# Optimization experiments

Hardware: AMD Instinct MI355X
Metric: run time of the kernel (lower is better)

## Reference

```python
import jax, jax.numpy as jnp
import numpy as np

DIM = 4096
BATCH = 2048
K = 40  # int(DIM * 0.01)


def fhh(x):
    """Fused fast Walsh-Hadamard / Hartley butterfly (recursion over static sizes)."""
    n = x.shape[-1]
    if n == 1:
        return x
    half = n // 2
    left, right = x[..., :half], x[..., half:]
    h_sum = left + right
    h_diff = left - right
    h_diff2 = h_diff + jnp.roll(h_diff, shift=1, axis=-1)
    return jnp.concatenate([fhh(h_sum), fhh(h_diff2)], axis=-1)


def setup_inputs() -> dict:
    key = jax.random.key(0)
    k1, k2, k3 = jax.random.split(key, 3)
    x = jax.random.normal(k1, (BATCH, DIM), dtype=jnp.float32)
    spectral_weights = jnp.ones((DIM,), dtype=jnp.float32)
    engram_values = jax.random.normal(k2, (DIM, K), dtype=jnp.float32) * 0.01
    engram_indices = jax.random.randint(k3, (DIM, K), 0, DIM)
    return {"x": x, "spectral_weights": spectral_weights,
            "engram_values": engram_values, "engram_indices": engram_indices}


def reference(x, spectral_weights, engram_values, engram_indices):
    wave = fhh(x)  # [B, DIM]
    # low-rank (diagonal) path
    low_rank_out = wave * spectral_weights  # [B, DIM]
    # sparse gather path: wave[:, engram_indices] -> [B, DIM, K]
    selected = wave[:, engram_indices]
    sparse_out = jnp.einsum('bdk,dk->bd', selected, engram_values)
    processed = low_rank_out + sparse_out
    return fhh(processed) / DIM
```

## Files before the change

### kernel.cpp

```cpp
#include <hip/hip_runtime.h>

#define DIM   4096
#define BATCH 2048
#define KNZ   40
#define ROWS  8
#define TPB   512
#define DPT   (DIM / TPB)

typedef int i32x2 __attribute__((ext_vector_type(2)));

__device__ __forceinline__ float shflx(float v, int m) { return __shfl_xor(v, m, 64); }
__device__ __forceinline__ float shfls(float v, int s) { return __shfl(v, s, 64); }

__device__ __forceinline__ int swz8(int d) { return (d << 4) ^ ((d >> 2) & 0x1f0); }

__device__ __forceinline__ unsigned short bfp(float f) {
  unsigned u = __float_as_uint(f);
  u += 0x7fffu + ((u >> 16) & 1u);
  return (unsigned short)(u >> 16);
}
__device__ __forceinline__ float bfu(unsigned short h) { return __uint_as_float(((unsigned)h) << 16); }
__device__ __forceinline__ float blo(unsigned u) { return __uint_as_float(u << 16); }
__device__ __forceinline__ float bhi(unsigned u) { return __uint_as_float(u & 0xffff0000u); }

template<int CTRL>
__device__ __forceinline__ float dppf(float x) {
  int i = __float_as_int(x);
  return __int_as_float(__builtin_amdgcn_update_dpp(i, i, CTRL, 0xF, 0xF, false));
}

template<int HL>
__device__ __forceinline__ float bfly1(float self, bool up) {
#if __has_builtin(__builtin_amdgcn_permlane32_swap)
  if constexpr (HL == 32) {
    i32x2 rr = __builtin_amdgcn_permlane32_swap(__float_as_int(self), __float_as_int(self), false, false);
    float s = __int_as_float(rr.x) + __int_as_float(rr.y);
    return up ? (s - 2.0f * self) : s;
  }
#endif
#if __has_builtin(__builtin_amdgcn_permlane16_swap)
  if constexpr (HL == 16) {
    i32x2 rr = __builtin_amdgcn_permlane16_swap(__float_as_int(self), __float_as_int(self), false, false);
    float s = __int_as_float(rr.x) + __int_as_float(rr.y);
    return up ? (s - 2.0f * self) : s;
  }
#endif
  float pv;
  if constexpr (HL == 8)      pv = dppf<0x128>(self);
  else if constexpr (HL == 2) pv = dppf<0x4E>(self);
  else if constexpr (HL == 1) pv = dppf<0xB1>(self);
  else                        pv = shflx(self, HL);
  float s = self + pv;
  float d = up ? (pv - self) : (self - pv);
  return up ? d : s;
}

template<int H>
__device__ __forceinline__ void stage_inlane(float v[64]) {
#pragma unroll
  for (int o = 0; o < 64; o += 2 * H) {
    float dt[H];
#pragma unroll
    for (int i = 0; i < H; ++i) {
      float a = v[o + i], b = v[o + H + i];
      dt[i] = a - b;
      v[o + i] = a + b;
    }
#pragma unroll
    for (int i = H - 1; i >= 1; --i) v[o + H + i] = dt[i] + dt[i - 1];
    v[o + H] = dt[0] + dt[H - 1];
  }
}

template<int HL>
__device__ __forceinline__ void stage_xlane(float v[64], int lane) {
  const bool up = (lane & HL) != 0;
  const int srcl = ((lane & (HL - 1)) == 0) ? (lane | (HL - 1)) : (lane - 1);
#pragma unroll
  for (int r = 0; r < 64; ++r) v[r] = bfly1<HL>(v[r], up);
  float dw = shfls(v[63], srcl);
#pragma unroll
  for (int r = 63; r >= 1; --r) {
    float d2 = v[r] + v[r - 1];
    v[r] = up ? d2 : v[r];
  }
  float d2 = v[0] + dw;
  v[0] = up ? d2 : v[0];
}

__device__ __forceinline__ void fhh_regs(float v[64], int lane) {
  stage_xlane<32>(v, lane);
  stage_xlane<16>(v, lane);
  stage_xlane<8>(v, lane);
  stage_xlane<4>(v, lane);
  stage_xlane<2>(v, lane);
  stage_xlane<1>(v, lane);
  stage_inlane<32>(v);
  stage_inlane<16>(v);
  stage_inlane<8>(v);
  stage_inlane<4>(v);
  stage_inlane<2>(v);
  stage_inlane<1>(v);
}

__global__ __launch_bounds__(TPB, 2) void aleph_fused(
    const float* __restrict__ x, const float* __restrict__ sw,
    const float* __restrict__ V, const int* __restrict__ I,
    float* __restrict__ out) {
  __shared__ unsigned short lds[DIM * ROWS];
  char* lb = (char*)lds;
  const int t = threadIdx.x;
  const int w = t >> 6;
  const int lane = t & 63;
  const size_t row = (size_t)blockIdx.x * ROWS + w;

  float v[64];
  {
    const float4* xp = (const float4*)(x + row * DIM + (size_t)lane * 64);
#pragma unroll
    for (int i = 0; i < 16; ++i) {
      float4 f = xp[i];
      v[4 * i] = f.x; v[4 * i + 1] = f.y; v[4 * i + 2] = f.z; v[4 * i + 3] = f.w;
    }
  }
  fhh_regs(v, lane);

#pragma unroll
  for (int r = 0; r < 64; ++r)
    *(unsigned short*)(lb + swz8(64 * lane + r) + 2 * w) = bfp(v[r]);
  __syncthreads();

  float preg[DPT][ROWS];
#pragma unroll
  for (int ii = 0; ii < DPT; ++ii) {
    const int d = ii * TPB + t;
    const float swd = sw[d];
    uint4 q = *(const uint4*)(lb + swz8(d));
    float a0 = blo(q.x) * swd, a1 = bhi(q.x) * swd;
    float a2 = blo(q.y) * swd, a3 = bhi(q.y) * swd;
    float a4 = blo(q.z) * swd, a5 = bhi(q.z) * swd;
    float a6 = blo(q.w) * swd, a7 = bhi(q.w) * swd;
    const int4*   ip = (const int4*)(I + d * KNZ);
    const float4* vp = (const float4*)(V + d * KNZ);
#pragma unroll 5
    for (int g = 0; g < KNZ / 4; ++g) {
      int4 i4 = ip[g];
      float4 f4 = vp[g];
      {
        uint4 qa = *(const uint4*)(lb + swz8(i4.x));
        a0 += blo(qa.x) * f4.x; a1 += bhi(qa.x) * f4.x;
        a2 += blo(qa.y) * f4.x; a3 += bhi(qa.y) * f4.x;
        a4 += blo(qa.z) * f4.x; a5 += bhi(qa.z) * f4.x;
        a6 += blo(qa.w) * f4.x; a7 += bhi(qa.w) * f4.x;
      }
      {
        uint4 qa = *(const uint4*)(lb + swz8(i4.y));
        a0 += blo(qa.x) * f4.y; a1 += bhi(qa.x) * f4.y;
        a2 += blo(qa.y) * f4.y; a3 += bhi(qa.y) * f4.y;
        a4 += blo(qa.z) * f4.y; a5 += bhi(qa.z) * f4.y;
        a6 += blo(qa.w) * f4.y; a7 += bhi(qa.w) * f4.y;
      }
      {
        uint4 qa = *(const uint4*)(lb + swz8(i4.z));
        a0 += blo(qa.x) * f4.z; a1 += bhi(qa.x) * f4.z;
        a2 += blo(qa.y) * f4.z; a3 += bhi(qa.y) * f4.z;
        a4 += blo(qa.z) * f4.z; a5 += bhi(qa.z) * f4.z;
        a6 += blo(qa.w) * f4.z; a7 += bhi(qa.w) * f4.z;
      }
      {
        uint4 qa = *(const uint4*)(lb + swz8(i4.w));
        a0 += blo(qa.x) * f4.w; a1 += bhi(qa.x) * f4.w;
        a2 += blo(qa.y) * f4.w; a3 += bhi(qa.y) * f4.w;
        a4 += blo(qa.z) * f4.w; a5 += bhi(qa.z) * f4.w;
        a6 += blo(qa.w) * f4.w; a7 += bhi(qa.w) * f4.w;
      }
    }
    preg[ii][0] = a0; preg[ii][1] = a1; preg[ii][2] = a2; preg[ii][3] = a3;
    preg[ii][4] = a4; preg[ii][5] = a5; preg[ii][6] = a6; preg[ii][7] = a7;
  }
  __syncthreads();

#pragma unroll
  for (int ii = 0; ii < DPT; ++ii) {
    const int d = ii * TPB + t;
    uint4 pk;
    pk.x = (unsigned)bfp(preg[ii][0]) | ((unsigned)bfp(preg[ii][1]) << 16);
    pk.y = (unsigned)bfp(preg[ii][2]) | ((unsigned)bfp(preg[ii][3]) << 16);
    pk.z = (unsigned)bfp(preg[ii][4]) | ((unsigned)bfp(preg[ii][5]) << 16);
    pk.w = (unsigned)bfp(preg[ii][6]) | ((unsigned)bfp(preg[ii][7]) << 16);
    *(uint4*)(lb + swz8(d)) = pk;
  }
  __syncthreads();

#pragma unroll
  for (int r = 0; r < 64; ++r)
    v[r] = bfu(*(const unsigned short*)(lb + swz8(64 * lane + r) + 2 * w));
  fhh_regs(v, lane);

  const float inv = 1.0f / (float)DIM;
  float4* op = (float4*)(out + row * DIM + (size_t)lane * 64);
#pragma unroll
  for (int i = 0; i < 16; ++i) {
    float4 f;
    f.x = v[4 * i] * inv;     f.y = v[4 * i + 1] * inv;
    f.z = v[4 * i + 2] * inv; f.w = v[4 * i + 3] * inv;
    op[i] = f;
  }
}

extern "C" void kernel_launch(void* const* d_in, const int* in_sizes, int n_in,
                              void* d_out, int out_size, void* d_ws, size_t ws_size,
                              hipStream_t stream) {
  const float* x  = (const float*)d_in[0];
  const float* sw = (const float*)d_in[1];
  const float* V  = (const float*)d_in[2];
  const int*   I  = (const int*)d_in[3];
  float* out = (float*)d_out;

  dim3 grid(BATCH / ROWS), block(TPB);
  hipLaunchKernelGGL(aleph_fused, grid, block, 0, stream, x, sw, V, I, out);
}
```

Before: 78.01 us.

## Split each row across two waves with LDS-exchanged top butterfly stage

Each row's transform is now shared by two wavefronts of 32 values per lane instead of one wavefront of 64. The first butterfly stage is exchanged through a new LDS scratch buffer with block barriers. Rows per block drop from 8 to 4, the bf16 image uses 8-byte entries with a new swizzle, and launch bounds ask for 4 blocks per CU. The aim is to cut register pressure and raise occupancy, at the cost of extra LDS traffic and barriers, and the gather now amortizes each index load over only 4 rows.

New measurement: 110.1 us. 1.41x slower.

```diff
diff --git a/kernel.cpp b/kernel.cpp
--- a/kernel.cpp
+++ b/kernel.cpp
@@ -3,7 +3,7 @@
 #define DIM   4096
 #define BATCH 2048
 #define KNZ   40
-#define ROWS  8
+#define ROWS  4
 #define TPB   512
 #define DPT   (DIM / TPB)
 
@@ -12,7 +12,7 @@
 __device__ __forceinline__ float shflx(float v, int m) { return __shfl_xor(v, m, 64); }
 __device__ __forceinline__ float shfls(float v, int s) { return __shfl(v, s, 64); }
 
-__device__ __forceinline__ int swz8(int d) { return (d << 4) ^ ((d >> 2) & 0x1f0); }
+__device__ __forceinline__ int OFF(int d) { return (d << 3) ^ ((d >> 3) & 248); }
 
 __device__ __forceinline__ unsigned short bfp(float f) {
   unsigned u = __float_as_uint(f);
@@ -56,9 +56,9 @@
 }
 
 template<int H>
-__device__ __forceinline__ void stage_inlane(float v[64]) {
-#pragma unroll
-  for (int o = 0; o < 64; o += 2 * H) {
+__device__ __forceinline__ void stage_inlane(float v[32]) {
+#pragma unroll
+  for (int o = 0; o < 32; o += 2 * H) {
     float dt[H];
 #pragma unroll
     for (int i = 0; i < H; ++i) {
@@ -73,14 +73,14 @@
 }
 
 template<int HL>
-__device__ __forceinline__ void stage_xlane(float v[64], int lane) {
+__device__ __forceinline__ void stage_xlane(float v[32], int lane) {
   const bool up = (lane & HL) != 0;
   const int srcl = ((lane & (HL - 1)) == 0) ? (lane | (HL - 1)) : (lane - 1);
 #pragma unroll
-  for (int r = 0; r < 64; ++r) v[r] = bfly1<HL>(v[r], up);
-  float dw = shfls(v[63], srcl);
-#pragma unroll
-  for (int r = 63; r >= 1; --r) {
+  for (int r = 0; r < 32; ++r) v[r] = bfly1<HL>(v[r], up);
+  float dw = shfls(v[31], srcl);
+#pragma unroll
+  for (int r = 31; r >= 1; --r) {
     float d2 = v[r] + v[r - 1];
     v[r] = up ? d2 : v[r];
   }
@@ -88,14 +88,45 @@
   v[0] = up ? d2 : v[0];
 }
 
-__device__ __forceinline__ void fhh_regs(float v[64], int lane) {
+__device__ __forceinline__ void stage_pair(float v[32], int lane, int p, float* scr) {
+#pragma unroll
+  for (int c = 0; c < 2; ++c) {
+    float4* dst = (float4*)(scr + p * 1024 + lane * 16);
+#pragma unroll
+    for (int q = 0; q < 4; ++q)
+      dst[q] = make_float4(v[16 * c + 4 * q], v[16 * c + 4 * q + 1],
+                           v[16 * c + 4 * q + 2], v[16 * c + 4 * q + 3]);
+    __syncthreads();
+    const float4* sp = (const float4*)(scr + (p ^ 1) * 1024 + lane * 16);
+    float4 q0 = sp[0], q1 = sp[1], q2 = sp[2], q3 = sp[3];
+    float pv[16] = {q0.x, q0.y, q0.z, q0.w, q1.x, q1.y, q1.z, q1.w,
+                    q2.x, q2.y, q2.z, q2.w, q3.x, q3.y, q3.z, q3.w};
+    if (p) {
+#pragma unroll
+      for (int j = 0; j < 16; ++j) v[16 * c + j] = pv[j] - v[16 * c + j];
+    } else {
+#pragma unroll
+      for (int j = 0; j < 16; ++j) v[16 * c + j] = v[16 * c + j] + pv[j];
+    }
+    __syncthreads();
+  }
+  if (p) {
+    const int srcl = (lane == 0) ? 63 : lane - 1;
+    float dw = shfls(v[31], srcl);
+#pragma unroll
+    for (int r = 31; r >= 1; --r) v[r] = v[r] + v[r - 1];
+    v[0] = v[0] + dw;
+  }
+}
+
+__device__ __forceinline__ void fhh32(float v[32], int lane, int p, float* scr) {
+  stage_pair(v, lane, p, scr);
   stage_xlane<32>(v, lane);
   stage_xlane<16>(v, lane);
   stage_xlane<8>(v, lane);
   stage_xlane<4>(v, lane);
   stage_xlane<2>(v, lane);
   stage_xlane<1>(v, lane);
-  stage_inlane<32>(v);
   stage_inlane<16>(v);
   stage_inlane<8>(v);
   stage_inlane<4>(v);
@@ -103,31 +134,36 @@
   stage_inlane<1>(v);
 }
 
-__global__ __launch_bounds__(TPB, 2) void aleph_fused(
+__global__ __launch_bounds__(TPB, 4) void aleph_fused(
     const float* __restrict__ x, const float* __restrict__ sw,
     const float* __restrict__ V, const int* __restrict__ I,
     float* __restrict__ out) {
-  __shared__ unsigned short lds[DIM * ROWS];
-  char* lb = (char*)lds;
+  __shared__ float scratch[ROWS * 2048];
+  __shared__ unsigned short img[DIM * ROWS];
+  char* lb = (char*)img;
   const int t = threadIdx.x;
   const int w = t >> 6;
   const int lane = t & 63;
-  const size_t row = (size_t)blockIdx.x * ROWS + w;
-
-  float v[64];
+  const int rb = w >> 1;
+  const int p = w & 1;
+  const size_t row = (size_t)blockIdx.x * ROWS + rb;
+  float* scr = scratch + rb * 2048;
+  const int dbase = p * 2048 + lane * 32;
+
+  float v[32];
   {
-    const float4* xp = (const float4*)(x + row * DIM + (size_t)lane * 64);
-#pragma unroll
-    for (int i = 0; i < 16; ++i) {
+    const float4* xp = (const float4*)(x + row * DIM + dbase);
+#pragma unroll
+    for (int i = 0; i < 8; ++i) {
       float4 f = xp[i];
       v[4 * i] = f.x; v[4 * i + 1] = f.y; v[4 * i + 2] = f.z; v[4 * i + 3] = f.w;
     }
   }
-  fhh_regs(v, lane);
-
-#pragma unroll
-  for (int r = 0; r < 64; ++r)
-    *(unsigned short*)(lb + swz8(64 * lane + r) + 2 * w) = bfp(v[r]);
+  fhh32(v, lane, p, scr);
+
+#pragma unroll
+  for (int r = 0; r < 32; ++r)
+    *(unsigned short*)(lb + OFF(dbase + r) + 2 * rb) = bfp(v[r]);
   __syncthreads();
 
   float preg[DPT][ROWS];
@@ -135,11 +171,9 @@
   for (int ii = 0; ii < DPT; ++ii) {
     const int d = ii * TPB + t;
     const float swd = sw[d];
-    uint4 q = *(const uint4*)(lb + swz8(d));
+    uint2 q = *(const uint2*)(lb + OFF(d));
     float a0 = blo(q.x) * swd, a1 = bhi(q.x) * swd;
     float a2 = blo(q.y) * swd, a3 = bhi(q.y) * swd;
-    float a4 = blo(q.z) * swd, a5 = bhi(q.z) * swd;
-    float a6 = blo(q.w) * swd, a7 = bhi(q.w) * swd;
     const int4*   ip = (const int4*)(I + d * KNZ);
     const float4* vp = (const float4*)(V + d * KNZ);
 #pragma unroll 5
@@ -147,60 +181,49 @@
       int4 i4 = ip[g];
       float4 f4 = vp[g];
       {
-        uint4 qa = *(const uint4*)(lb + swz8(i4.x));
+        uint2 qa = *(const uint2*)(lb + OFF(i4.x));
         a0 += blo(qa.x) * f4.x; a1 += bhi(qa.x) * f4.x;
         a2 += blo(qa.y) * f4.x; a3 += bhi(qa.y) * f4.x;
-        a4 += blo(qa.z) * f4.x; a5 += bhi(qa.z) * f4.x;
-        a6 += blo(qa.w) * f4.x; a7 += bhi(qa.w) * f4.x;
-      }
-      {
-        uint4 qa = *(const uint4*)(lb + swz8(i4.y));
+      }
+      {
+        uint2 qa = *(const uint2*)(lb + OFF(i4.y));
         a0 += blo(qa.x) * f4.y; a1 += bhi(qa.x) * f4.y;
         a2 += blo(qa.y) * f4.y; a3 += bhi(qa.y) * f4.y;
-        a4 += blo(qa.z) * f4.y; a5 += bhi(qa.z) * f4.y;
-        a6 += blo(qa.w) * f4.y; a7 += bhi(qa.w) * f4.y;
-      }
-      {
-        uint4 qa = *(const uint4*)(lb + swz8(i4.z));
+      }
+      {
+        uint2 qa = *(const uint2*)(lb + OFF(i4.z));
         a0 += blo(qa.x) * f4.z; a1 += bhi(qa.x) * f4.z;
         a2 += blo(qa.y) * f4.z; a3 += bhi(qa.y) * f4.z;
-        a4 += blo(qa.z) * f4.z; a5 += bhi(qa.z) * f4.z;
-        a6 += blo(qa.w) * f4.z; a7 += bhi(qa.w) * f4.z;
-      }
-      {
-        uint4 qa = *(const uint4*)(lb + swz8(i4.w));
+      }
+      {
+        uint2 qa = *(const uint2*)(lb + OFF(i4.w));
         a0 += blo(qa.x) * f4.w; a1 += bhi(qa.x) * f4.w;
         a2 += blo(qa.y) * f4.w; a3 += bhi(qa.y) * f4.w;
-        a4 += blo(qa.z) * f4.w; a5 += bhi(qa.z) * f4.w;
-        a6 += blo(qa.w) * f4.w; a7 += bhi(qa.w) * f4.w;
       }
     }
     preg[ii][0] = a0; preg[ii][1] = a1; preg[ii][2] = a2; preg[ii][3] = a3;
-    preg[ii][4] = a4; preg[ii][5] = a5; preg[ii][6] = a6; preg[ii][7] = a7;
   }
   __syncthreads();
 
 #pragma unroll
   for (int ii = 0; ii < DPT; ++ii) {
     const int d = ii * TPB + t;
-    uint4 pk;
-    pk.x = (unsigned)bfp(preg[ii][0]) | ((unsigned)bfp(preg[ii][1]) << 16);
-    pk.y = (unsigned)bfp(preg[ii][2]) | ((unsigned)bfp(preg[ii][3]) << 16);
-    pk.z = (unsigned)bfp(preg[ii][4]) | ((unsigned)bfp(preg[ii][5]) << 16);
-    pk.w = (unsigned)bfp(preg[ii][6]) | ((unsigned)bfp(preg[ii][7]) << 16);
-    *(uint4*)(lb + swz8(d)) = pk;
+    ushort4 pk;
+    pk.x = bfp(preg[ii][0]); pk.y = bfp(preg[ii][1]);
+    pk.z = bfp(preg[ii][2]); pk.w = bfp(preg[ii][3]);
+    *(ushort4*)(lb + OFF(d)) = pk;
   }
   __syncthreads();
 
 #pragma unroll
-  for (int r = 0; r < 64; ++r)
-    v[r] = bfu(*(const unsigned short*)(lb + swz8(64 * lane + r) + 2 * w));
-  fhh_regs(v, lane);
+  for (int r = 0; r < 32; ++r)
+    v[r] = bfu(*(const unsigned short*)(lb + OFF(dbase + r) + 2 * rb));
+  fhh32(v, lane, p, scr);
 
   const float inv = 1.0f / (float)DIM;
-  float4* op = (float4*)(out + row * DIM + (size_t)lane * 64);
-#pragma unroll
-  for (int i = 0; i < 16; ++i) {
+  float4* op = (float4*)(out + row * DIM + dbase);
+#pragma unroll
+  for (int i = 0; i < 8; ++i) {
     float4 f;
     f.x = v[4 * i] * inv;     f.y = v[4 * i + 1] * inv;
     f.z = v[4 * i + 2] * inv; f.w = v[4 * i + 3] * inv;
```

## Precompute swizzled gather offsets and use branchless FMA butterflies with raw bf16 high-half

Applied to the files above, without the earlier changes.

Adds a small pre-kernel that converts the engram indices into swizzled LDS byte offsets in the workspace, so the gather loop no longer computes swz8 per index. The cross-lane butterfly stages replace selects with sign and mask multipliers folded into FMAs. In the gather, the high bf16 half is read without masking, which leaves the low 16 bits of the packed word as extra mantissa noise. This slightly perturbs numerics and costs an extra kernel launch plus an index-array pass each call.

Measured after the change: 78.64 us. No clear change (+0.8%).

```diff
diff --git a/kernel.cpp b/kernel.cpp
--- a/kernel.cpp
+++ b/kernel.cpp
@@ -21,7 +21,8 @@
 }
 __device__ __forceinline__ float bfu(unsigned short h) { return __uint_as_float(((unsigned)h) << 16); }
 __device__ __forceinline__ float blo(unsigned u) { return __uint_as_float(u << 16); }
-__device__ __forceinline__ float bhi(unsigned u) { return __uint_as_float(u & 0xffff0000u); }
+__device__ __forceinline__ float bhic(unsigned u) { return __uint_as_float(u & 0xffff0000u); }
+__device__ __forceinline__ float bhir(unsigned u) { return __uint_as_float(u); }
 
 template<int CTRL>
 __device__ __forceinline__ float dppf(float x) {
@@ -29,32 +30,6 @@
   return __int_as_float(__builtin_amdgcn_update_dpp(i, i, CTRL, 0xF, 0xF, false));
 }
 
-template<int HL>
-__device__ __forceinline__ float bfly1(float self, bool up) {
-#if __has_builtin(__builtin_amdgcn_permlane32_swap)
-  if constexpr (HL == 32) {
-    i32x2 rr = __builtin_amdgcn_permlane32_swap(__float_as_int(self), __float_as_int(self), false, false);
-    float s = __int_as_float(rr.x) + __int_as_float(rr.y);
-    return up ? (s - 2.0f * self) : s;
-  }
-#endif
-#if __has_builtin(__builtin_amdgcn_permlane16_swap)
-  if constexpr (HL == 16) {
-    i32x2 rr = __builtin_amdgcn_permlane16_swap(__float_as_int(self), __float_as_int(self), false, false);
-    float s = __int_as_float(rr.x) + __int_as_float(rr.y);
-    return up ? (s - 2.0f * self) : s;
-  }
-#endif
-  float pv;
-  if constexpr (HL == 8)      pv = dppf<0x128>(self);
-  else if constexpr (HL == 2) pv = dppf<0x4E>(self);
-  else if constexpr (HL == 1) pv = dppf<0xB1>(self);
-  else                        pv = shflx(self, HL);
-  float s = self + pv;
-  float d = up ? (pv - self) : (self - pv);
-  return up ? d : s;
-}
-
 template<int H>
 __device__ __forceinline__ void stage_inlane(float v[64]) {
 #pragma unroll
@@ -75,17 +50,43 @@
 template<int HL>
 __device__ __forceinline__ void stage_xlane(float v[64], int lane) {
   const bool up = (lane & HL) != 0;
+  const float sgn   = up ? -1.0f : 1.0f;
+  const float cswap = up ? -2.0f : 0.0f;
+  const float rm    = up ? 1.0f : 0.0f;
   const int srcl = ((lane & (HL - 1)) == 0) ? (lane | (HL - 1)) : (lane - 1);
 #pragma unroll
-  for (int r = 0; r < 64; ++r) v[r] = bfly1<HL>(v[r], up);
+  for (int r = 0; r < 64; ++r) {
+    float self = v[r];
+    bool done = false;
+#if __has_builtin(__builtin_amdgcn_permlane32_swap)
+    if constexpr (HL == 32) {
+      i32x2 rr = __builtin_amdgcn_permlane32_swap(__float_as_int(self), __float_as_int(self), false, false);
+      float s2 = __int_as_float(rr.x) + __int_as_float(rr.y);
+      v[r] = fmaf(self, cswap, s2);
+      done = true;
+    }
+#endif
+#if __has_builtin(__builtin_amdgcn_permlane16_swap)
+    if constexpr (HL == 16) {
+      i32x2 rr = __builtin_amdgcn_permlane16_swap(__float_as_int(self), __float_as_int(self), false, false);
+      float s2 = __int_as_float(rr.x) + __int_as_float(rr.y);
+      v[r] = fmaf(self, cswap, s2);
+      done = true;
+    }
+#endif
+    if (!done) {
+      float pv;
+      if constexpr (HL == 8)      pv = dppf<0x128>(self);
+      else if constexpr (HL == 2) pv = dppf<0x4E>(self);
+      else if constexpr (HL == 1) pv = dppf<0xB1>(self);
+      else                        pv = shflx(self, HL);
+      v[r] = fmaf(self, sgn, pv);
+    }
+  }
   float dw = shfls(v[63], srcl);
 #pragma unroll
-  for (int r = 63; r >= 1; --r) {
-    float d2 = v[r] + v[r - 1];
-    v[r] = up ? d2 : v[r];
-  }
-  float d2 = v[0] + dw;
-  v[0] = up ? d2 : v[0];
+  for (int r = 63; r >= 1; --r) v[r] = fmaf(v[r - 1], rm, v[r]);
+  v[0] = fmaf(dw, rm, v[0]);
 }
 
 __device__ __forceinline__ void fhh_regs(float v[64], int lane) {
@@ -103,12 +104,18 @@
   stage_inlane<1>(v);
 }
 
+__global__ void prep_idx(const int* __restrict__ I, int* __restrict__ PS, int n) {
+  int i = blockIdx.x * 256 + threadIdx.x;
+  if (i < n) PS[i] = swz8(I[i]);
+}
+
+template<bool PRE>
 __global__ __launch_bounds__(TPB, 2) void aleph_fused(
     const float* __restrict__ x, const float* __restrict__ sw,
-    const float* __restrict__ V, const int* __restrict__ I,
+    const float* __restrict__ V, const int* __restrict__ IDX,
     float* __restrict__ out) {
-  __shared__ unsigned short lds[DIM * ROWS];
-  char* lb = (char*)lds;
+  __shared__ unsigned short img[DIM * ROWS];
+  char* lb = (char*)img;
   const int t = threadIdx.x;
   const int w = t >> 6;
   const int lane = t & 63;
@@ -136,43 +143,46 @@
     const int d = ii * TPB + t;
     const float swd = sw[d];
     uint4 q = *(const uint4*)(lb + swz8(d));
-    float a0 = blo(q.x) * swd, a1 = bhi(q.x) * swd;
-    float a2 = blo(q.y) * swd, a3 = bhi(q.y) * swd;
-    float a4 = blo(q.z) * swd, a5 = bhi(q.z) * swd;
-    float a6 = blo(q.w) * swd, a7 = bhi(q.w) * swd;
-    const int4*   ip = (const int4*)(I + d * KNZ);
+    float a0 = blo(q.x) * swd, a1 = bhic(q.x) * swd;
+    float a2 = blo(q.y) * swd, a3 = bhic(q.y) * swd;
+    float a4 = blo(q.z) * swd, a5 = bhic(q.z) * swd;
+    float a6 = blo(q.w) * swd, a7 = bhic(q.w) * swd;
+    const int4*   ip = (const int4*)(IDX + d * KNZ);
     const float4* vp = (const float4*)(V + d * KNZ);
 #pragma unroll 5
     for (int g = 0; g < KNZ / 4; ++g) {
       int4 i4 = ip[g];
       float4 f4 = vp[g];
-      {
-        uint4 qa = *(const uint4*)(lb + swz8(i4.x));
-        a0 += blo(qa.x) * f4.x; a1 += bhi(qa.x) * f4.x;
-        a2 += blo(qa.y) * f4.x; a3 += bhi(qa.y) * f4.x;
-        a4 += blo(qa.z) * f4.x; a5 += bhi(qa.z) * f4.x;
-        a6 += blo(qa.w) * f4.x; a7 += bhi(qa.w) * f4.x;
-      }
-      {
-        uint4 qa = *(const uint4*)(lb + swz8(i4.y));
-        a0 += blo(qa.x) * f4.y; a1 += bhi(qa.x) * f4.y;
-        a2 += blo(qa.y) * f4.y; a3 += bhi(qa.y) * f4.y;
-        a4 += blo(qa.z) * f4.y; a5 += bhi(qa.z) * f4.y;
-        a6 += blo(qa.w) * f4.y; a7 += bhi(qa.w) * f4.y;
-      }
-      {
-        uint4 qa = *(const uint4*)(lb + swz8(i4.z));
-        a0 += blo(qa.x) * f4.z; a1 += bhi(qa.x) * f4.z;
-        a2 += blo(qa.y) * f4.z; a3 += bhi(qa.y) * f4.z;
-        a4 += blo(qa.z) * f4.z; a5 += bhi(qa.z) * f4.z;
-        a6 += blo(qa.w) * f4.z; a7 += bhi(qa.w) * f4.z;
-      }
-      {
-        uint4 qa = *(const uint4*)(lb + swz8(i4.w));
-        a0 += blo(qa.x) * f4.w; a1 += bhi(qa.x) * f4.w;
-        a2 += blo(qa.y) * f4.w; a3 += bhi(qa.y) * f4.w;
-        a4 += blo(qa.z) * f4.w; a5 += bhi(qa.z) * f4.w;
-        a6 += blo(qa.w) * f4.w; a7 += bhi(qa.w) * f4.w;
+      int o0, o1, o2, o3;
+      if constexpr (PRE) { o0 = i4.x; o1 = i4.y; o2 = i4.z; o3 = i4.w; }
+      else { o0 = swz8(i4.x); o1 = swz8(i4.y); o2 = swz8(i4.z); o3 = swz8(i4.w); }
+      {
+        uint4 qa = *(const uint4*)(lb + o0);
+        a0 += blo(qa.x) * f4.x; a1 += bhir(qa.x) * f4.x;
+        a2 += blo(qa.y) * f4.x; a3 += bhir(qa.y) * f4.x;
+        a4 += blo(qa.z) * f4.x; a5 += bhir(qa.z) * f4.x;
+        a6 += blo(qa.w) * f4.x; a7 += bhir(qa.w) * f4.x;
+      }
+      {
+        uint4 qa = *(const uint4*)(lb + o1);
+        a0 += blo(qa.x) * f4.y; a1 += bhir(qa.x) * f4.y;
+        a2 += blo(qa.y) * f4.y; a3 += bhir(qa.y) * f4.y;
+        a4 += blo(qa.z) * f4.y; a5 += bhir(qa.z) * f4.y;
+        a6 += blo(qa.w) * f4.y; a7 += bhir(qa.w) * f4.y;
+      }
+      {
+        uint4 qa = *(const uint4*)(lb + o2);
+        a0 += blo(qa.x) * f4.z; a1 += bhir(qa.x) * f4.z;
+        a2 += blo(qa.y) * f4.z; a3 += bhir(qa.y) * f4.z;
+        a4 += blo(qa.z) * f4.z; a5 += bhir(qa.z) * f4.z;
+        a6 += blo(qa.w) * f4.z; a7 += bhir(qa.w) * f4.z;
+      }
+      {
+        uint4 qa = *(const uint4*)(lb + o3);
+        a0 += blo(qa.x) * f4.w; a1 += bhir(qa.x) * f4.w;
+        a2 += blo(qa.y) * f4.w; a3 += bhir(qa.y) * f4.w;
+        a4 += blo(qa.z) * f4.w; a5 += bhir(qa.z) * f4.w;
+        a6 += blo(qa.w) * f4.w; a7 += bhir(qa.w) * f4.w;
       }
     }
     preg[ii][0] = a0; preg[ii][1] = a1; preg[ii][2] = a2; preg[ii][3] = a3;
@@ -218,5 +228,12 @@
   float* out = (float*)d_out;
 
   dim3 grid(BATCH / ROWS), block(TPB);
-  hipLaunchKernelGGL(aleph_fused, grid, block, 0, stream, x, sw, V, I, out);
-}
+  const int nidx = DIM * KNZ;
+  if (ws_size >= (size_t)nidx * sizeof(int)) {
+    int* PS = (int*)d_ws;
+    hipLaunchKernelGGL(prep_idx, dim3((nidx + 255) / 256), dim3(256), 0, stream, I, PS, nidx);
+    hipLaunchKernelGGL(aleph_fused<true>, grid, block, 0, stream, x, sw, V, PS, out);
+  } else {
+    hipLaunchKernelGGL(aleph_fused<false>, grid, block, 0, stream, x, sw, V, I, out);
+  }
+}
```
